# Kernel optimization log

Measured on AMD Instinct MI355X. Metric: run time of the kernel, lower is better.

## Reference

```python
import jax, jax.numpy as jnp
import numpy as np

B, T, D, H, L = 4, 2048, 256, 4, 2
HD = D // H
VOCAB, MAX_BITS, MLP_H = 32, 64, 64


def setup_inputs() -> dict:
    key = jax.random.key(0)
    ks = jax.random.split(key, 20)
    s = 0.02
    n = lambda k, shp: (jax.random.normal(k, shp, jnp.float32) * s)
    inp = {
        'tokens': jax.random.randint(ks[0], (B, T), 0, VOCAB),
        'embed': n(ks[1], (VOCAB, D)),
        'ln1_w': jnp.ones((L, D)), 'ln1_b': jnp.zeros((L, D)),
        'qkv_w': n(ks[2], (L, D, 3 * D)), 'qkv_b': jnp.zeros((L, 3 * D)),
        'proj_w': n(ks[3], (L, D, D)), 'proj_b': jnp.zeros((L, D)),
        'ln2_w': jnp.ones((L, D)), 'ln2_b': jnp.zeros((L, D)),
        'ffn1_w': n(ks[4], (L, D, 4 * D)), 'ffn1_b': jnp.zeros((L, 4 * D)),
        'ffn2_w': n(ks[5], (L, 4 * D, D)), 'ffn2_b': jnp.zeros((L, D)),
        'lnf_w': jnp.ones((D,)), 'lnf_b': jnp.zeros((D,)),
        'out_queries': n(ks[6], (MAX_BITS * 2, D)),
        'outp_w': n(ks[7], (D, 1)), 'outp_b': jnp.zeros((1,)),
        'mlp_w1': n(ks[8], (3, MLP_H)), 'mlp_b1': jnp.zeros((MLP_H,)),
        'mlp_w2': n(ks[9], (MLP_H, MLP_H)), 'mlp_b2': jnp.zeros((MLP_H,)),
        'mlp_w3': n(ks[10], (MLP_H, 2)), 'mlp_b3': jnp.zeros((2,)),
    }
    return inp


def _layernorm(x, w, b, eps=1e-5):
    mu = jnp.mean(x, axis=-1, keepdims=True)
    var = jnp.mean(jnp.square(x - mu), axis=-1, keepdims=True)
    return (x - mu) * jax.lax.rsqrt(var + eps) * w + b


def _rope_tables(t_len, hd):
    inv_freq = 1.0 / (10000.0 ** (jnp.arange(0, hd, 2, dtype=jnp.float32) / hd))
    freqs = jnp.outer(jnp.arange(t_len, dtype=jnp.float32), inv_freq)  # [T, hd/2]
    emb = jnp.concatenate([freqs, freqs], axis=-1)                     # [T, hd]
    return jnp.cos(emb)[None, :, None, :], jnp.sin(emb)[None, :, None, :]


def _rotate_half(x):
    x1, x2 = x[..., : x.shape[-1] // 2], x[..., x.shape[-1] // 2:]
    return jnp.concatenate([-x2, x1], axis=-1)


def _attention(x, qkv_w, qkv_b, proj_w, proj_b):
    b, t, c = x.shape
    qkv = (x @ qkv_w + qkv_b).reshape(b, t, 3, H, HD)
    q, k, v = qkv[:, :, 0], qkv[:, :, 1], qkv[:, :, 2]  # [B,T,H,HD]
    cos, sin = _rope_tables(t, HD)
    q = q * cos + _rotate_half(q) * sin
    k = k * cos + _rotate_half(k) * sin
    scores = jnp.einsum('bthd,bshd->bhts', q, k) / jnp.sqrt(jnp.float32(HD))
    causal = jnp.tril(jnp.ones((t, t), dtype=bool))
    scores = jnp.where(causal, scores, -jnp.inf)
    attn = jax.nn.softmax(scores, axis=-1)
    out = jnp.einsum('bhts,bshd->bthd', attn, v).reshape(b, t, c)
    return out @ proj_w + proj_b


def reference(tokens, embed, ln1_w, ln1_b, qkv_w, qkv_b, proj_w, proj_b,
              ln2_w, ln2_b, ffn1_w, ffn1_b, ffn2_w, ffn2_b, lnf_w, lnf_b,
              out_queries, outp_w, outp_b,
              mlp_w1, mlp_b1, mlp_w2, mlp_b2, mlp_w3, mlp_b3):
    x = embed[tokens]  # [B,T,D]
    for l in range(L):
        x = x + _attention(_layernorm(x, ln1_w[l], ln1_b[l]),
                           qkv_w[l], qkv_b[l], proj_w[l], proj_b[l])
        h = _layernorm(x, ln2_w[l], ln2_b[l])
        h = jax.nn.gelu(h @ ffn1_w[l] + ffn1_b[l], approximate=False)
        x = x + (h @ ffn2_w[l] + ffn2_b[l])
    x = _layernorm(x, lnf_w, lnf_b)
    # query cross-attention for bit-pair selection
    q_scores = jnp.einsum('qd,btd->bqt', out_queries, x) / jnp.sqrt(jnp.float32(D))
    q_attn = jax.nn.softmax(q_scores, axis=-1)           # [B, 2*MAX_BITS, T]
    selected = jnp.einsum('bqt,btd->bqd', q_attn, x)
    bits = jax.nn.sigmoid((selected @ outp_w + outp_b)[..., 0])
    pairs = bits.reshape(-1, MAX_BITS, 2)                # [B, MAX_BITS, 2]

    # sequential full-adder over bits
    def step(carry, ab):  # carry [B], ab [B,2]
        z = jnp.concatenate([ab, carry[:, None]], axis=-1)  # [B,3]
        h = jax.nn.relu(z @ mlp_w1 + mlp_b1)
        h = jax.nn.relu(h @ mlp_w2 + mlp_b2)
        o = jax.nn.sigmoid(h @ mlp_w3 + mlp_b3)
        return o[:, 1], o[:, 0]

    carry0 = jnp.zeros((pairs.shape[0],), jnp.float32)
    carry, sum_bits = jax.lax.scan(step, carry0, jnp.swapaxes(pairs, 0, 1))
    sum_all = jnp.concatenate([sum_bits.T, carry[:, None]], axis=1)  # [B, MAX_BITS+1]
    return sum_all, pairs, q_attn
```

## Files before the change

### kernel.cpp

```cpp
#include <hip/hip_runtime.h>
#include <hip/hip_bf16.h>

#define BB 4
#define TT 2048
#define DD 256
#define HH 4
#define HDD 64
#define NROW 8192
#define NQ 128

typedef __hip_bfloat16 bf16;
typedef __attribute__((ext_vector_type(8))) short bf8v;
typedef __attribute__((ext_vector_type(4))) short bf4v;
typedef __attribute__((ext_vector_type(4))) float f4v;

__device__ __forceinline__ bf16 f2b(float v){ return __float2bfloat16(v); }
__device__ __forceinline__ short f2bs(float v){
    bf16 h = __float2bfloat16(v);
    return *reinterpret_cast<short*>(&h);
}
__device__ __forceinline__ float bs2f(short s){
    bf16 h = *reinterpret_cast<bf16*>(&s);
    return __bfloat162float(h);
}
__device__ __forceinline__ float rl(float v, int l){
    return __uint_as_float(__builtin_amdgcn_readlane(__float_as_uint(v), l));
}

#define DPP_ROR_ADD(v, ctrl) \
    ((v) + __int_as_float(__builtin_amdgcn_update_dpp(0, __float_as_int(v), (ctrl), 0xF, 0xF, false)))

__device__ __forceinline__ float swap16_add(float v){
    float a = v, b = v;
    asm("v_permlane16_swap_b32 %0, %1" : "+v"(a), "+v"(b));
    return a + b;
}
__device__ __forceinline__ float swap32_add(float v){
    float a = v, b = v;
    asm("v_permlane32_swap_b32 %0, %1" : "+v"(a), "+v"(b));
    return a + b;
}

#define MFMA32(A,B,C) __builtin_amdgcn_mfma_f32_16x16x32_bf16((A),(B),(C),0,0,0)
#if __has_builtin(__builtin_amdgcn_mfma_f32_16x16x16bf16_1k)
#define MFMA16(A,B,C) __builtin_amdgcn_mfma_f32_16x16x16bf16_1k((A),(B),(C),0,0,0)
#else
__device__ __forceinline__ f4v mfma16_asm(bf4v a, bf4v b, f4v c){
    f4v d;
    asm("v_mfma_f32_16x16x16_bf16 %0, %1, %2, %3" : "=v"(d) : "v"(a), "v"(b), "v"(c));
    return d;
}
#define MFMA16(A,B,C) mfma16_asm((A),(B),(C))
#endif

__global__ __launch_bounds__(256) void k_embln(const int* __restrict__ tok,
                                               const float* __restrict__ emb,
                                               const float* __restrict__ w,
                                               const float* __restrict__ b,
                                               float* __restrict__ x,
                                               bf16* __restrict__ Y){
    __shared__ float red[256];
    int n = blockIdx.x, d = threadIdx.x;
    float v = emb[(long)tok[n]*DD + d];
    x[(long)n*DD + d] = v;
    red[d] = v; __syncthreads();
    for (int s=128; s>0; s>>=1){ if (d<s) red[d]+=red[d+s]; __syncthreads(); }
    float mu = red[0] * (1.0f/DD); __syncthreads();
    float df = v - mu;
    red[d] = df*df; __syncthreads();
    for (int s=128; s>0; s>>=1){ if (d<s) red[d]+=red[d+s]; __syncthreads(); }
    float var = red[0] * (1.0f/DD);
    Y[(long)n*DD + d] = f2b(df*rsqrtf(var+1e-5f)*w[d] + b[d]);
}

__global__ __launch_bounds__(256) void k_misc(const float* __restrict__ oq, bf16* __restrict__ oqb,
                                              float* __restrict__ cosT, float* __restrict__ sinT,
                                              const float* __restrict__ w2, float* __restrict__ w2t){
    int gid = blockIdx.x*256 + threadIdx.x;
    {
        int t = gid >> 5, dd = gid & 31;
        float invf = powf(10000.0f, -(float)(2*dd)/64.0f);
        float ang = (float)t * invf;
        float sn, cs;
        sincosf(ang, &sn, &cs);
        cosT[gid] = cs; sinT[gid] = sn;
    }
    if (gid < NQ*DD) oqb[gid] = f2b(oq[gid]);
    if (gid < 4096){ int j = gid >> 6, k = gid & 63; w2t[gid] = w2[k*64 + j]; }
}

__global__ __launch_bounds__(256) void k_wtall(const float* __restrict__ qkvw,
                                               const float* __restrict__ projw,
                                               const float* __restrict__ f1w,
                                               const float* __restrict__ f2w,
                                               bf16* __restrict__ wt){
    __shared__ float t[32][33];
    int z = blockIdx.z;
    int l = z >> 2, type = z & 3;
    long L = (long)l*786432;
    int K, M; const float* src; long doff;
    if (type == 0){ K=256;  M=768;  src = qkvw + (long)l*256*768;  doff = L; }
    else if (type == 1){ K=256;  M=256;  src = projw + (long)l*256*256; doff = L + 196608; }
    else if (type == 2){ K=256;  M=1024; src = f1w  + (long)l*256*1024; doff = L + 262144; }
    else               { K=1024; M=256;  src = f2w  + (long)l*1024*256; doff = L + 524288; }
    int m0 = blockIdx.x*32, k0 = blockIdx.y*32;
    if (m0 >= M || k0 >= K) return;
    bf16* dst = wt + doff;
    int tx = threadIdx.x, ty = threadIdx.y;
    #pragma unroll
    for (int i=0;i<4;i++)
        t[ty+i*8][tx] = src[(long)(k0+ty+i*8)*M + m0 + tx];
    __syncthreads();
    #pragma unroll
    for (int i=0;i<4;i++)
        dst[(long)(m0+ty+i*8)*K + k0 + tx] = f2b(t[tx][ty+i*8]);
}

__global__ __launch_bounds__(256) void k_lnb(const float* __restrict__ X,
                                             const float* __restrict__ w,
                                             const float* __restrict__ b,
                                             bf16* __restrict__ Y){
    __shared__ float red[256];
    int n = blockIdx.x, d = threadIdx.x;
    float v = X[(long)n*DD + d];
    red[d] = v; __syncthreads();
    for (int s=128; s>0; s>>=1){ if (d<s) red[d]+=red[d+s]; __syncthreads(); }
    float mu = red[0] * (1.0f/DD); __syncthreads();
    float df = v - mu;
    red[d] = df*df; __syncthreads();
    for (int s=128; s>0; s>>=1){ if (d<s) red[d]+=red[d+s]; __syncthreads(); }
    float var = red[0] * (1.0f/DD);
    Y[(long)n*DD + d] = f2b(df*rsqrtf(var+1e-5f)*w[d] + b[d]);
}

__global__ __launch_bounds__(256) void k_lnf(const float* __restrict__ X,
                                             const float* __restrict__ w,
                                             const float* __restrict__ b,
                                             const float* __restrict__ ow,
                                             bf16* __restrict__ Yb,
                                             float* __restrict__ g){
    __shared__ float red[256];
    int n = blockIdx.x, d = threadIdx.x;
    float v = X[(long)n*DD + d];
    red[d] = v; __syncthreads();
    for (int s=128; s>0; s>>=1){ if (d<s) red[d]+=red[d+s]; __syncthreads(); }
    float mu = red[0] * (1.0f/DD); __syncthreads();
    float df = v - mu;
    red[d] = df*df; __syncthreads();
    for (int s=128; s>0; s>>=1){ if (d<s) red[d]+=red[d+s]; __syncthreads(); }
    float var = red[0] * (1.0f/DD);
    float y = df*rsqrtf(var+1e-5f)*w[d] + b[d];
    Yb[(long)n*DD + d] = f2b(y);
    __syncthreads();
    red[d] = y * ow[d]; __syncthreads();
    for (int s=128; s>0; s>>=1){ if (d<s) red[d]+=red[d+s]; __syncthreads(); }
    if (d == 0) g[n] = red[0];
}

__global__ __launch_bounds__(256) void k_mgemm(const bf16* __restrict__ A,
                                               const bf16* __restrict__ Wt,
                                               const float* __restrict__ bias,
                                               float* __restrict__ Cf,
                                               bf16* __restrict__ Cb,
                                               int K, int M, int mode){
    __shared__ short As[128*32];
    __shared__ short Ws[64*32];
    int tid = threadIdx.x;
    int lane = tid & 63, wv = tid >> 6;
    int n0 = blockIdx.y * 128, m0 = blockIdx.x * 64;
    int rbase = (wv >> 1) * 64, cbase = (wv & 1) * 32;
    f4v acc[4][2] = {};
    int s2 = tid + 256;
    for (int k0 = 0; k0 < K; k0 += 32){
        bf8v va0 = *(const bf8v*)(A  + (long)(n0 + (tid>>2))*K + k0 + ((tid&3)<<3));
        bf8v va1 = *(const bf8v*)(A  + (long)(n0 + (s2 >>2))*K + k0 + ((s2 &3)<<3));
        bf8v vw  = *(const bf8v*)(Wt + (long)(m0 + (tid>>2))*K + k0 + ((tid&3)<<3));
        __syncthreads();
        *(bf8v*)&As[tid*8] = va0;
        *(bf8v*)&As[s2 *8] = va1;
        *(bf8v*)&Ws[tid*8] = vw;
        __syncthreads();
        bf8v af[4], bfr[2];
        int k8 = (lane >> 4) << 3;
        #pragma unroll
        for (int i=0;i<4;i++) af[i]  = *(bf8v*)&As[(rbase + i*16 + (lane&15))*32 + k8];
        #pragma unroll
        for (int j=0;j<2;j++) bfr[j] = *(bf8v*)&Ws[(cbase + j*16 + (lane&15))*32 + k8];
        #pragma unroll
        for (int i=0;i<4;i++)
            #pragma unroll
            for (int j=0;j<2;j++)
                acc[i][j] = MFMA32(af[i], bfr[j], acc[i][j]);
    }
    int rq = (lane >> 4) * 4;
    int cl = lane & 15;
    #pragma unroll
    for (int i=0;i<4;i++){
        #pragma unroll
        for (int j=0;j<2;j++){
            int m = m0 + cbase + j*16 + cl;
            float bs = bias[m];
            #pragma unroll
            for (int r=0;r<4;r++){
                int n = n0 + rbase + i*16 + rq + r;
                float v = acc[i][j][r] + bs;
                long idx = (long)n*M + m;
                if (mode == 0)      Cf[idx] = v;
                else if (mode == 1) Cf[idx] += v;
                else if (mode == 2) Cb[idx] = f2b(0.5f*v*(1.0f + erff(v*0.70710678118654752f)));
                else                Cb[idx] = f2b(v);
            }
        }
    }
}

__global__ __launch_bounds__(256) void k_mgemmQKV(const bf16* __restrict__ A,
                                                  const bf16* __restrict__ Wt,
                                                  const float* __restrict__ bias,
                                                  const float* __restrict__ cosT,
                                                  const float* __restrict__ sinT,
                                                  bf16* __restrict__ qb,
                                                  bf16* __restrict__ kb,
                                                  bf16* __restrict__ vt){
    __shared__ short As[128*32];
    __shared__ short Ws[64*32];
    __shared__ short E[128][68];
    const int K = 256, M = 768;
    int tid = threadIdx.x;
    int lane = tid & 63, wv = tid >> 6;
    int n0 = blockIdx.y * 128, m0 = blockIdx.x * 64;
    int rbase = (wv >> 1) * 64, cbase = (wv & 1) * 32;
    f4v acc[4][2] = {};
    int s2 = tid + 256;
    for (int k0 = 0; k0 < K; k0 += 32){
        bf8v va0 = *(const bf8v*)(A  + (long)(n0 + (tid>>2))*K + k0 + ((tid&3)<<3));
        bf8v va1 = *(const bf8v*)(A  + (long)(n0 + (s2 >>2))*K + k0 + ((s2 &3)<<3));
        bf8v vw  = *(const bf8v*)(Wt + (long)(m0 + (tid>>2))*K + k0 + ((tid&3)<<3));
        __syncthreads();
        *(bf8v*)&As[tid*8] = va0;
        *(bf8v*)&As[s2 *8] = va1;
        *(bf8v*)&Ws[tid*8] = vw;
        __syncthreads();
        bf8v af[4], bfr[2];
        int k8 = (lane >> 4) << 3;
        #pragma unroll
        for (int i=0;i<4;i++) af[i]  = *(bf8v*)&As[(rbase + i*16 + (lane&15))*32 + k8];
        #pragma unroll
        for (int j=0;j<2;j++) bfr[j] = *(bf8v*)&Ws[(cbase + j*16 + (lane&15))*32 + k8];
        #pragma unroll
        for (int i=0;i<4;i++)
            #pragma unroll
            for (int j=0;j<2;j++)
                acc[i][j] = MFMA32(af[i], bfr[j], acc[i][j]);
    }
    int rq = (lane >> 4) * 4;
    int cl = lane & 15;
    #pragma unroll
    for (int i=0;i<4;i++){
        #pragma unroll
        for (int j=0;j<2;j++){
            int cc = cbase + j*16 + cl;
            float bs = bias[m0 + cc];
            #pragma unroll
            for (int r=0;r<4;r++)
                E[rbase + i*16 + rq + r][cc] = f2bs(acc[i][j][r] + bs);
        }
    }
    __syncthreads();
    int part = m0 >> 8;
    int h = (m0 >> 6) & 3;
    int b = n0 >> 11;
    int t0 = n0 & 2047;
    int bh = b*HH + h;
    if (part < 2){
        bf16* dst0 = part ? kb : qb;
        int r2 = tid >> 2;
        int c0 = (tid & 3) * 16;
        int cpx = c0 ^ 32;
        #pragma unroll
        for (int half=0; half<2; half++){
            int row = half*64 + r2;
            int t = t0 + row;
            bf8v e0 = *(bf8v*)&E[row][c0];
            bf8v e1 = *(bf8v*)&E[row][c0+8];
            bf8v p0 = *(bf8v*)&E[row][cpx];
            bf8v p1 = *(bf8v*)&E[row][cpx+8];
            const float* ct = cosT + t*32;
            const float* st = sinT + t*32;
            short o[16];
            #pragma unroll
            for (int i=0;i<8;i++){
                int d = c0 + i, dd = d & 31;
                float cs = ct[dd], sn = st[dd];
                float v = bs2f(e0[i]), v2 = bs2f(p0[i]);
                o[i] = f2bs((d < 32) ? (v*cs - v2*sn) : (v*cs + v2*sn));
            }
            #pragma unroll
            for (int i=0;i<8;i++){
                int d = c0 + 8 + i, dd = d & 31;
                float cs = ct[dd], sn = st[dd];
                float v = bs2f(e1[i]), v2 = bs2f(p1[i]);
                o[8+i] = f2bs((d < 32) ? (v*cs - v2*sn) : (v*cs + v2*sn));
            }
            short* dp = (short*)dst0 + ((long)bh*TT + t)*64 + c0;
            *(bf8v*)dp     = *(bf8v*)&o[0];
            *(bf8v*)(dp+8) = *(bf8v*)&o[8];
        }
    } else {
        int tIdx0 = t0 >> 6;
        int d  = (tid & 127) >> 1;
        int k0 = (tid & 1) * 32;
        int tt = tid >> 7;
        short o[32];
        #pragma unroll
        for (int k=0;k<32;k++) o[k] = E[tt*64 + k0 + k][d];
        short* dp = (short*)vt + (((long)bh*32 + tIdx0 + tt)*64 + d)*64 + k0;
        *(bf8v*)dp      = *(bf8v*)&o[0];
        *(bf8v*)(dp+8)  = *(bf8v*)&o[8];
        *(bf8v*)(dp+16) = *(bf8v*)&o[16];
        *(bf8v*)(dp+24) = *(bf8v*)&o[24];
    }
}

__global__ __launch_bounds__(256) void k_fattn(const bf16* __restrict__ qb,
                                               const bf16* __restrict__ kb,
                                               const bf16* __restrict__ vt,
                                               bf16* __restrict__ ob){
    __shared__ short Ks[2][64][72];
    __shared__ short Vs[2][64][68];
    int bh = blockIdx.y;
    int qt = (int)(gridDim.x - 1) - (int)blockIdx.x;
    int tid = threadIdx.x;
    int lane = tid & 63, w = tid >> 6;
    int col = lane & 15, quad = lane >> 4;
    int q0 = qt*64 + w*16;
    const bf16* qp = qb + ((long)bh*TT + q0 + col)*64 + quad*8;
    bf8v bq0 = *(const bf8v*)(qp);
    bf8v bq1 = *(const bf8v*)(qp + 32);
    f4v oc[4] = {};
    float lsum = 0.f;
    int qglob = q0 + col;
    int srow = tid >> 2, sc0 = (tid & 3) * 16;
    const short* kgb = (const short*)kb + ((long)bh*TT + srow)*64 + sc0;
    const short* vgb = (const short*)vt + (((long)bh*32)*64 + srow)*64 + sc0;

    bf8v pk0 = *(const bf8v*)kgb;
    bf8v pk1 = *(const bf8v*)(kgb + 8);
    bf8v pv0 = *(const bf8v*)vgb;
    bf8v pv1 = *(const bf8v*)(vgb + 8);
    *(bf8v*)&Ks[0][srow][sc0]     = pk0;
    *(bf8v*)&Ks[0][srow][sc0 + 8] = pk1;
    *(bf8v*)&Vs[0][srow][sc0]     = pv0;
    *(bf8v*)&Vs[0][srow][sc0 + 8] = pv1;

    int buf = 0;
    for (int kt=0; kt<=qt; kt++){
        __syncthreads();
        bool more = (kt < qt);
        if (more){
            const short* kg = kgb + (long)(kt+1)*4096;
            const short* vg = vgb + (long)(kt+1)*4096;
            pk0 = *(const bf8v*)kg;
            pk1 = *(const bf8v*)(kg + 8);
            pv0 = *(const bf8v*)vg;
            pv1 = *(const bf8v*)(vg + 8);
        }
        bool diag = (kt == qt);
        int ntmax = diag ? w : 3;
        bf4v bp[4];
        #pragma unroll
        for (int nt=0; nt<4; nt++){
            if (nt > ntmax) continue;
            bf8v ka0 = *(const bf8v*)&Ks[buf][nt*16 + col][quad*8];
            bf8v ka1 = *(const bf8v*)&Ks[buf][nt*16 + col][32 + quad*8];
            f4v st = {};
            st = MFMA32(ka0, bq0, st);
            st = MFMA32(ka1, bq1, st);
            int key0 = kt*64 + nt*16 + quad*4;
            bf4v pb;
            #pragma unroll
            for (int r=0; r<4; r++){
                float e = __expf(st[r]*0.125f);
                if (diag && (key0 + r > qglob)) e = 0.f;
                lsum += e;
                pb[r] = f2bs(e);
            }
            bp[nt] = pb;
        }
        #pragma unroll
        for (int dt=0; dt<4; dt++){
            #pragma unroll
            for (int nt=0; nt<4; nt++){
                if (nt > ntmax) continue;
                bf4v va = *(const bf4v*)&Vs[buf][dt*16 + col][nt*16 + quad*4];
                oc[dt] = MFMA16(va, bp[nt], oc[dt]);
            }
        }
        if (more){
            *(bf8v*)&Ks[buf^1][srow][sc0]     = pk0;
            *(bf8v*)&Ks[buf^1][srow][sc0 + 8] = pk1;
            *(bf8v*)&Vs[buf^1][srow][sc0]     = pv0;
            *(bf8v*)&Vs[buf^1][srow][sc0 + 8] = pv1;
        }
        buf ^= 1;
    }
    lsum += __shfl_xor(lsum, 16, 64);
    lsum += __shfl_xor(lsum, 32, 64);
    float linv = 1.0f / lsum;

    int b = bh / HH, h = bh % HH;
    long obase = ((long)b*TT + q0 + col)*DD + h*64 + quad*4;
    #pragma unroll
    for (int dt=0; dt<4; dt++){
        bf4v o4;
        #pragma unroll
        for (int r=0; r<4; r++) o4[r] = f2bs(oc[dt][r]*linv);
        *(bf4v*)(ob + obase + dt*16) = o4;
    }
}

__global__ __launch_bounds__(256) void k_score(const bf16* __restrict__ oqb,
                                               const bf16* __restrict__ xfb,
                                               float* __restrict__ S){
    int b = blockIdx.y, t0 = blockIdx.x*64;
    int tid = threadIdx.x, lane = tid & 63, w = tid >> 6;
    int col = lane & 15, quad = lane >> 4, k8 = quad << 3;
    const bf16* xb = xfb + (long)b*TT*DD;
    f4v acc[2][4] = {};
    #pragma unroll
    for (int ko=0; ko<8; ko++){
        int kk = ko*32 + k8;
        bf8v a0 = *(const bf8v*)(oqb + (long)(w*32 +      col)*DD + kk);
        bf8v a1 = *(const bf8v*)(oqb + (long)(w*32 + 16 + col)*DD + kk);
        #pragma unroll
        for (int bt=0; bt<4; bt++){
            bf8v bv = *(const bf8v*)(xb + (long)(t0 + bt*16 + col)*DD + kk);
            acc[0][bt] = MFMA32(a0, bv, acc[0][bt]);
            acc[1][bt] = MFMA32(a1, bv, acc[1][bt]);
        }
    }
    #pragma unroll
    for (int qt2=0; qt2<2; qt2++){
        #pragma unroll
        for (int bt=0; bt<4; bt++){
            #pragma unroll
            for (int r=0; r<4; r++){
                int q = w*32 + qt2*16 + quad*4 + r;
                S[((long)b*NQ + q)*TT + t0 + bt*16 + col] = acc[qt2][bt][r]*0.0625f;
            }
        }
    }
}

__global__ __launch_bounds__(256) void k_psoft(const float* __restrict__ S,
                                               const float* __restrict__ g,
                                               const float* __restrict__ obias,
                                               float* __restrict__ out_qattn,
                                               float* __restrict__ out_pairs,
                                               float* __restrict__ bits){
    __shared__ float p[TT];
    __shared__ float red[256];
    int bq = blockIdx.x, b = bq >> 7;
    int tid = threadIdx.x;
    const float* Srow = S + (long)bq*TT;
    float lmax = -1e30f;
    for (int t=tid; t<TT; t+=256){ float s = Srow[t]; p[t] = s; lmax = fmaxf(lmax, s); }
    red[tid] = lmax; __syncthreads();
    for (int s2=128; s2>0; s2>>=1){ if (tid<s2) red[tid]=fmaxf(red[tid],red[tid+s2]); __syncthreads(); }
    float m = red[0]; __syncthreads();
    const float* gb = g + (long)b*TT;
    float lsum = 0.f, gdot = 0.f;
    for (int t=tid; t<TT; t+=256){
        float e = __expf(p[t]-m); p[t] = e;
        lsum += e; gdot += e*gb[t];
    }
    red[tid] = lsum; __syncthreads();
    for (int s2=128; s2>0; s2>>=1){ if (tid<s2) red[tid]+=red[tid+s2]; __syncthreads(); }
    float inv = 1.0f/red[0]; __syncthreads();
    red[tid] = gdot; __syncthreads();
    for (int s2=128; s2>0; s2>>=1){ if (tid<s2) red[tid]+=red[tid+s2]; __syncthreads(); }
    float gsum = red[0];
    for (int t=tid; t<TT; t+=256) out_qattn[(long)bq*TT + t] = p[t]*inv;
    if (tid == 0){
        float bit = 1.0f/(1.0f + expf(-(gsum*inv + obias[0])));
        bits[bq] = bit;
        out_pairs[bq] = bit;
    }
}

__global__ __launch_bounds__(64) void k_scan(const float* __restrict__ bits,
                                             const float* __restrict__ w1, const float* __restrict__ b1,
                                             const float* __restrict__ w2t, const float* __restrict__ b2,
                                             const float* __restrict__ w3, const float* __restrict__ b3,
                                             float* __restrict__ out_sum){
    __shared__ __align__(16) float h1s[64];
    int b = blockIdx.x, lane = threadIdx.x;
    float w1c0 = w1[lane], w1c1 = w1[64 + lane], w1c2 = w1[128 + lane];
    float b1v = b1[lane], b2v = b2[lane];
    float w3c0 = w3[lane*2 + 0], w3c1 = w3[lane*2 + 1];
    float b30 = b3[0], b31 = b3[1];
    const f4v* wrow = (const f4v*)(w2t + (long)lane*64);
    f4v c0v = wrow[0],  c1v = wrow[1],  c2v = wrow[2],  c3v = wrow[3],
        c4v = wrow[4],  c5v = wrow[5],  c6v = wrow[6],  c7v = wrow[7],
        c8v = wrow[8],  c9v = wrow[9],  cav = wrow[10], cbv = wrow[11],
        ccv = wrow[12], cdv = wrow[13], cev = wrow[14], cfv = wrow[15];
    float z0v = bits[b*128 + lane*2 + 0];
    float z1v = bits[b*128 + lane*2 + 1];
    const f4v* hv = (const f4v*)h1s;
    float carry = 0.f;
    for (int step=0; step<64; step++){
        float z0 = rl(z0v, step);
        float z1 = rl(z1v, step);
        float h1 = fmaxf(z0*w1c0 + z1*w1c1 + carry*w1c2 + b1v, 0.f);
        h1s[lane] = h1;
        __syncthreads();
        f4v va = hv[0]*c0v,  vb = hv[1]*c1v,  vc = hv[2]*c2v,   vd = hv[3]*c3v;
        va += hv[4]*c4v;   vb += hv[5]*c5v;   vc += hv[6]*c6v;   vd += hv[7]*c7v;
        va += hv[8]*c8v;   vb += hv[9]*c9v;   vc += hv[10]*cav;  vd += hv[11]*cbv;
        va += hv[12]*ccv;  vb += hv[13]*cdv;  vc += hv[14]*cev;  vd += hv[15]*cfv;
        __syncthreads();
        f4v vs = (va + vb) + (vc + vd);
        float h2 = fmaxf(((vs[0] + vs[1]) + (vs[2] + vs[3])) + b2v, 0.f);
        float t0 = h2*w3c0, t1 = h2*w3c1;
        t0 = DPP_ROR_ADD(t0, 0x121); t1 = DPP_ROR_ADD(t1, 0x121);
        t0 = DPP_ROR_ADD(t0, 0x122); t1 = DPP_ROR_ADD(t1, 0x122);
        t0 = DPP_ROR_ADD(t0, 0x124); t1 = DPP_ROR_ADD(t1, 0x124);
        t0 = DPP_ROR_ADD(t0, 0x128); t1 = DPP_ROR_ADD(t1, 0x128);
        t0 = swap16_add(t0); t1 = swap16_add(t1);
        t0 = swap32_add(t0); t1 = swap32_add(t1);
        float o0 = 1.0f/(1.0f + __expf(-(t0 + b30)));
        carry    = 1.0f/(1.0f + __expf(-(t1 + b31)));
        if (lane == 0) out_sum[b*65 + step] = o0;
    }
    if (lane == 0) out_sum[b*65 + 64] = carry;
}

extern "C" void kernel_launch(void* const* d_in, const int* in_sizes, int n_in,
                              void* d_out, int out_size, void* d_ws, size_t ws_size,
                              hipStream_t stream){
    const int*   tok   = (const int*)d_in[0];
    const float* emb   = (const float*)d_in[1];
    const float* ln1w  = (const float*)d_in[2];
    const float* ln1b  = (const float*)d_in[3];
    const float* qkvw  = (const float*)d_in[4];
    const float* qkvb  = (const float*)d_in[5];
    const float* projw = (const float*)d_in[6];
    const float* projb = (const float*)d_in[7];
    const float* ln2w  = (const float*)d_in[8];
    const float* ln2b  = (const float*)d_in[9];
    const float* f1w   = (const float*)d_in[10];
    const float* f1b   = (const float*)d_in[11];
    const float* f2w   = (const float*)d_in[12];
    const float* f2bb  = (const float*)d_in[13];
    const float* lnfw  = (const float*)d_in[14];
    const float* lnfb  = (const float*)d_in[15];
    const float* oq    = (const float*)d_in[16];
    const float* ow    = (const float*)d_in[17];
    const float* obias = (const float*)d_in[18];
    const float* w1    = (const float*)d_in[19];
    const float* b1    = (const float*)d_in[20];
    const float* w2    = (const float*)d_in[21];
    const float* b2    = (const float*)d_in[22];
    const float* w3    = (const float*)d_in[23];
    const float* b3    = (const float*)d_in[24];
    float* out = (float*)d_out;

    const long MB = 1048576;
    char* W = (char*)d_ws;
    float* x     = (float*)(W);
    bf16*  attnb = (bf16*)(W + 8*MB);
    bf16*  hb    = (bf16*)(W + 16*MB);
    bf16*  qb    = (bf16*)(W + 32*MB);
    bf16*  kb    = (bf16*)(W + 36*MB);
    bf16*  vt    = (bf16*)(W + 44*MB);
    bf16*  xnb   = (bf16*)(W + 48*MB);
    bf16*  wt    = (bf16*)(W + 52*MB);
    float* bits  = (float*)(W + 55*MB);
    bf16*  oqb   = (bf16*)(W + 56*MB);
    float* cosT  = (float*)(W + 57*MB);
    float* sinT  = cosT + 65536;
    float* w2t   = (float*)(W + 58*MB);
    bf16*  xfb   = (bf16*)(W + 32*MB);
    float* g     = (float*)(W + 36*MB);
    float* S     = (float*)(W + 40*MB);

    k_wtall<<<dim3(32, 32, 8), dim3(32,8), 0, stream>>>(qkvw, projw, f1w, f2w, wt);
    k_misc<<<256, 256, 0, stream>>>(oq, oqb, cosT, sinT, w2, w2t);

    k_embln<<<NROW, 256, 0, stream>>>(tok, emb, ln1w, ln1b, x, xnb);
    for (int l=0; l<2; l++){
        long L = (long)l*786432;
        if (l) k_lnb<<<NROW, 256, 0, stream>>>(x, ln1w + l*DD, ln1b + l*DD, xnb);
        k_mgemmQKV<<<dim3(768/64, 64), 256, 0, stream>>>(
            xnb, wt + L, qkvb + l*768, cosT, sinT, qb, kb, vt);
        k_fattn<<<dim3(TT/64, BB*HH), 256, 0, stream>>>(qb, kb, vt, attnb);
        k_mgemm<<<dim3(256/64, 64), 256, 0, stream>>>(
            attnb, wt + L + 196608, projb + l*DD, x, (bf16*)0, 256, 256, 1);
        k_lnb<<<NROW, 256, 0, stream>>>(x, ln2w + l*DD, ln2b + l*DD, xnb);
        k_mgemm<<<dim3(1024/64, 64), 256, 0, stream>>>(
            xnb, wt + L + 262144, f1b + l*1024, (float*)0, hb, 256, 1024, 2);
        k_mgemm<<<dim3(256/64, 64), 256, 0, stream>>>(
            hb, wt + L + 524288, f2bb + l*DD, x, (bf16*)0, 1024, 256, 1);
    }
    k_lnf<<<NROW, 256, 0, stream>>>(x, lnfw, lnfb, ow, xfb, g);
    k_score<<<dim3(TT/64, BB), 256, 0, stream>>>(oqb, xfb, S);
    k_psoft<<<BB*NQ, 256, 0, stream>>>(S, g, obias, out + 772, out + 260, bits);
    k_scan<<<4, 64, 0, stream>>>(bits, w1, b1, w2t, b2, w3, b3, out);
}
```

Before: 433.5 us.

## Replace shared-memory tree reductions with wave-level DPP reductions in LN and softmax

Rewrites the layernorm kernels to process one row per wavefront, using 4-wide vector loads and DPP/permlane wave reductions, with variance computed as E[x^2]-mu^2 in a single pass. This replaces the 256-thread block reductions and their many __syncthreads. The pooled softmax keeps the row in registers and reduces with wave primitives plus a small cross-wave shared array. The scan kernel double-buffers its hidden-state buffer so one barrier per step can be dropped. The one-pass variance formula is slightly less numerically robust than the two-pass version.

```diff
diff --git a/kernel.cpp b/kernel.cpp
--- a/kernel.cpp
+++ b/kernel.cpp
@@ -13,6 +13,7 @@
 typedef __attribute__((ext_vector_type(8))) short bf8v;
 typedef __attribute__((ext_vector_type(4))) short bf4v;
 typedef __attribute__((ext_vector_type(4))) float f4v;
+typedef __attribute__((ext_vector_type(2))) unsigned int u2v;
 
 __device__ __forceinline__ bf16 f2b(float v){ return __float2bfloat16(v); }
 __device__ __forceinline__ short f2bs(float v){
@@ -29,16 +30,44 @@
 
 #define DPP_ROR_ADD(v, ctrl) \
     ((v) + __int_as_float(__builtin_amdgcn_update_dpp(0, __float_as_int(v), (ctrl), 0xF, 0xF, false)))
-
-__device__ __forceinline__ float swap16_add(float v){
-    float a = v, b = v;
+#define DPP_ROR_MAX(v, ctrl) \
+    fmaxf((v), __int_as_float(__builtin_amdgcn_update_dpp(0, __float_as_int(v), (ctrl), 0xF, 0xF, false)))
+
+__device__ __forceinline__ void plswap16(float v, float& a, float& b){
+#if __has_builtin(__builtin_amdgcn_permlane16_swap)
+    u2v r = __builtin_amdgcn_permlane16_swap(__float_as_uint(v), __float_as_uint(v), false, false);
+    a = __uint_as_float(r.x); b = __uint_as_float(r.y);
+#else
+    a = v; b = v;
+    asm volatile("" : "+v"(b));
     asm("v_permlane16_swap_b32 %0, %1" : "+v"(a), "+v"(b));
-    return a + b;
-}
-__device__ __forceinline__ float swap32_add(float v){
-    float a = v, b = v;
+#endif
+}
+__device__ __forceinline__ void plswap32(float v, float& a, float& b){
+#if __has_builtin(__builtin_amdgcn_permlane32_swap)
+    u2v r = __builtin_amdgcn_permlane32_swap(__float_as_uint(v), __float_as_uint(v), false, false);
+    a = __uint_as_float(r.x); b = __uint_as_float(r.y);
+#else
+    a = v; b = v;
+    asm volatile("" : "+v"(b));
     asm("v_permlane32_swap_b32 %0, %1" : "+v"(a), "+v"(b));
-    return a + b;
+#endif
+}
+__device__ __forceinline__ float swap16_add(float v){ float a,b; plswap16(v,a,b); return a + b; }
+__device__ __forceinline__ float swap32_add(float v){ float a,b; plswap32(v,a,b); return a + b; }
+__device__ __forceinline__ float swap16_max(float v){ float a,b; plswap16(v,a,b); return fmaxf(a,b); }
+__device__ __forceinline__ float swap32_max(float v){ float a,b; plswap32(v,a,b); return fmaxf(a,b); }
+__device__ __forceinline__ float wsum(float v){
+    v = DPP_ROR_ADD(v, 0x121); v = DPP_ROR_ADD(v, 0x122);
+    v = DPP_ROR_ADD(v, 0x124); v = DPP_ROR_ADD(v, 0x128);
+    v = swap16_add(v); v = swap32_add(v);
+    return v;
+}
+__device__ __forceinline__ float wmax(float v){
+    v = DPP_ROR_MAX(v, 0x121); v = DPP_ROR_MAX(v, 0x122);
+    v = DPP_ROR_MAX(v, 0x124); v = DPP_ROR_MAX(v, 0x128);
+    v = swap16_max(v); v = swap32_max(v);
+    return v;
 }
 
 #define MFMA32(A,B,C) __builtin_amdgcn_mfma_f32_16x16x32_bf16((A),(B),(C),0,0,0)
@@ -59,18 +88,22 @@
                                                const float* __restrict__ b,
                                                float* __restrict__ x,
                                                bf16* __restrict__ Y){
-    __shared__ float red[256];
-    int n = blockIdx.x, d = threadIdx.x;
-    float v = emb[(long)tok[n]*DD + d];
-    x[(long)n*DD + d] = v;
-    red[d] = v; __syncthreads();
-    for (int s=128; s>0; s>>=1){ if (d<s) red[d]+=red[d+s]; __syncthreads(); }
-    float mu = red[0] * (1.0f/DD); __syncthreads();
-    float df = v - mu;
-    red[d] = df*df; __syncthreads();
-    for (int s=128; s>0; s>>=1){ if (d<s) red[d]+=red[d+s]; __syncthreads(); }
-    float var = red[0] * (1.0f/DD);
-    Y[(long)n*DD + d] = f2b(df*rsqrtf(var+1e-5f)*w[d] + b[d]);
+    int row = blockIdx.x*4 + (threadIdx.x >> 6);
+    int lane = threadIdx.x & 63;
+    f4v v = *(const f4v*)(emb + (long)tok[row]*DD + lane*4);
+    *(f4v*)(x + (long)row*DD + lane*4) = v;
+    float s  = (v[0]+v[1]) + (v[2]+v[3]);
+    float s2 = (v[0]*v[0]+v[1]*v[1]) + (v[2]*v[2]+v[3]*v[3]);
+    s = wsum(s); s2 = wsum(s2);
+    float mu  = s * (1.0f/DD);
+    float var = s2 * (1.0f/DD) - mu*mu;
+    float rs  = rsqrtf(var + 1e-5f);
+    f4v wv4 = *(const f4v*)(w + lane*4);
+    f4v bv4 = *(const f4v*)(b + lane*4);
+    bf4v o;
+    #pragma unroll
+    for (int i=0;i<4;i++) o[i] = f2bs((v[i]-mu)*rs*wv4[i] + bv4[i]);
+    *(bf4v*)(Y + (long)row*DD + lane*4) = o;
 }
 
 __global__ __launch_bounds__(256) void k_misc(const float* __restrict__ oq, bf16* __restrict__ oqb,
@@ -120,17 +153,21 @@
                                              const float* __restrict__ w,
                                              const float* __restrict__ b,
                                              bf16* __restrict__ Y){
-    __shared__ float red[256];
-    int n = blockIdx.x, d = threadIdx.x;
-    float v = X[(long)n*DD + d];
-    red[d] = v; __syncthreads();
-    for (int s=128; s>0; s>>=1){ if (d<s) red[d]+=red[d+s]; __syncthreads(); }
-    float mu = red[0] * (1.0f/DD); __syncthreads();
-    float df = v - mu;
-    red[d] = df*df; __syncthreads();
-    for (int s=128; s>0; s>>=1){ if (d<s) red[d]+=red[d+s]; __syncthreads(); }
-    float var = red[0] * (1.0f/DD);
-    Y[(long)n*DD + d] = f2b(df*rsqrtf(var+1e-5f)*w[d] + b[d]);
+    int row = blockIdx.x*4 + (threadIdx.x >> 6);
+    int lane = threadIdx.x & 63;
+    f4v v = *(const f4v*)(X + (long)row*DD + lane*4);
+    float s  = (v[0]+v[1]) + (v[2]+v[3]);
+    float s2 = (v[0]*v[0]+v[1]*v[1]) + (v[2]*v[2]+v[3]*v[3]);
+    s = wsum(s); s2 = wsum(s2);
+    float mu  = s * (1.0f/DD);
+    float var = s2 * (1.0f/DD) - mu*mu;
+    float rs  = rsqrtf(var + 1e-5f);
+    f4v wv4 = *(const f4v*)(w + lane*4);
+    f4v bv4 = *(const f4v*)(b + lane*4);
+    bf4v o;
+    #pragma unroll
+    for (int i=0;i<4;i++) o[i] = f2bs((v[i]-mu)*rs*wv4[i] + bv4[i]);
+    *(bf4v*)(Y + (long)row*DD + lane*4) = o;
 }
 
 __global__ __launch_bounds__(256) void k_lnf(const float* __restrict__ X,
@@ -139,22 +176,29 @@
                                              const float* __restrict__ ow,
                                              bf16* __restrict__ Yb,
                                              float* __restrict__ g){
-    __shared__ float red[256];
-    int n = blockIdx.x, d = threadIdx.x;
-    float v = X[(long)n*DD + d];
-    red[d] = v; __syncthreads();
-    for (int s=128; s>0; s>>=1){ if (d<s) red[d]+=red[d+s]; __syncthreads(); }
-    float mu = red[0] * (1.0f/DD); __syncthreads();
-    float df = v - mu;
-    red[d] = df*df; __syncthreads();
-    for (int s=128; s>0; s>>=1){ if (d<s) red[d]+=red[d+s]; __syncthreads(); }
-    float var = red[0] * (1.0f/DD);
-    float y = df*rsqrtf(var+1e-5f)*w[d] + b[d];
-    Yb[(long)n*DD + d] = f2b(y);
-    __syncthreads();
-    red[d] = y * ow[d]; __syncthreads();
-    for (int s=128; s>0; s>>=1){ if (d<s) red[d]+=red[d+s]; __syncthreads(); }
-    if (d == 0) g[n] = red[0];
+    int row = blockIdx.x*4 + (threadIdx.x >> 6);
+    int lane = threadIdx.x & 63;
+    f4v v = *(const f4v*)(X + (long)row*DD + lane*4);
+    float s  = (v[0]+v[1]) + (v[2]+v[3]);
+    float s2 = (v[0]*v[0]+v[1]*v[1]) + (v[2]*v[2]+v[3]*v[3]);
+    s = wsum(s); s2 = wsum(s2);
+    float mu  = s * (1.0f/DD);
+    float var = s2 * (1.0f/DD) - mu*mu;
+    float rs  = rsqrtf(var + 1e-5f);
+    f4v wv4 = *(const f4v*)(w + lane*4);
+    f4v bv4 = *(const f4v*)(b + lane*4);
+    f4v ov4 = *(const f4v*)(ow + lane*4);
+    bf4v o;
+    float gp = 0.f;
+    #pragma unroll
+    for (int i=0;i<4;i++){
+        float y = (v[i]-mu)*rs*wv4[i] + bv4[i];
+        o[i] = f2bs(y);
+        gp += y * ov4[i];
+    }
+    *(bf4v*)(Yb + (long)row*DD + lane*4) = o;
+    gp = wsum(gp);
+    if (lane == 0) g[row] = gp;
 }
 
 __global__ __launch_bounds__(256) void k_mgemm(const bf16* __restrict__ A,
@@ -458,31 +502,36 @@
                                                float* __restrict__ out_qattn,
                                                float* __restrict__ out_pairs,
                                                float* __restrict__ bits){
-    __shared__ float p[TT];
-    __shared__ float red[256];
+    __shared__ float cmax[4], cs[4], cg[4];
     int bq = blockIdx.x, b = bq >> 7;
-    int tid = threadIdx.x;
-    const float* Srow = S + (long)bq*TT;
-    float lmax = -1e30f;
-    for (int t=tid; t<TT; t+=256){ float s = Srow[t]; p[t] = s; lmax = fmaxf(lmax, s); }
-    red[tid] = lmax; __syncthreads();
-    for (int s2=128; s2>0; s2>>=1){ if (tid<s2) red[tid]=fmaxf(red[tid],red[tid+s2]); __syncthreads(); }
-    float m = red[0]; __syncthreads();
-    const float* gb = g + (long)b*TT;
-    float lsum = 0.f, gdot = 0.f;
-    for (int t=tid; t<TT; t+=256){
-        float e = __expf(p[t]-m); p[t] = e;
-        lsum += e; gdot += e*gb[t];
-    }
-    red[tid] = lsum; __syncthreads();
-    for (int s2=128; s2>0; s2>>=1){ if (tid<s2) red[tid]+=red[tid+s2]; __syncthreads(); }
-    float inv = 1.0f/red[0]; __syncthreads();
-    red[tid] = gdot; __syncthreads();
-    for (int s2=128; s2>0; s2>>=1){ if (tid<s2) red[tid]+=red[tid+s2]; __syncthreads(); }
-    float gsum = red[0];
-    for (int t=tid; t<TT; t+=256) out_qattn[(long)bq*TT + t] = p[t]*inv;
+    int tid = threadIdx.x, wv = tid >> 6, lane = tid & 63;
+    const f4v* S4 = (const f4v*)(S + (long)bq*TT);
+    f4v s0 = S4[tid], s1 = S4[tid + 256];
+    float lmax = fmaxf(fmaxf(fmaxf(s0[0],s0[1]), fmaxf(s0[2],s0[3])),
+                       fmaxf(fmaxf(s1[0],s1[1]), fmaxf(s1[2],s1[3])));
+    lmax = wmax(lmax);
+    if (lane == 0) cmax[wv] = lmax;
+    __syncthreads();
+    float m = fmaxf(fmaxf(cmax[0],cmax[1]), fmaxf(cmax[2],cmax[3]));
+    const f4v* g4 = (const f4v*)(g + (long)b*TT);
+    f4v gv0 = g4[tid], gv1 = g4[tid + 256];
+    f4v e0, e1;
+    #pragma unroll
+    for (int i=0;i<4;i++){ e0[i] = __expf(s0[i]-m); e1[i] = __expf(s1[i]-m); }
+    float lsum = (e0[0]+e0[1]+e0[2]+e0[3]) + (e1[0]+e1[1]+e1[2]+e1[3]);
+    float gdot = (e0[0]*gv0[0]+e0[1]*gv0[1]+e0[2]*gv0[2]+e0[3]*gv0[3])
+               + (e1[0]*gv1[0]+e1[1]*gv1[1]+e1[2]*gv1[2]+e1[3]*gv1[3]);
+    lsum = wsum(lsum); gdot = wsum(gdot);
+    if (lane == 0){ cs[wv] = lsum; cg[wv] = gdot; }
+    __syncthreads();
+    float Lr = (cs[0]+cs[1]) + (cs[2]+cs[3]);
+    float G  = (cg[0]+cg[1]) + (cg[2]+cg[3]);
+    float inv = 1.0f / Lr;
+    f4v* out4 = (f4v*)(out_qattn + (long)bq*TT);
+    out4[tid]       = e0 * inv;
+    out4[tid + 256] = e1 * inv;
     if (tid == 0){
-        float bit = 1.0f/(1.0f + expf(-(gsum*inv + obias[0])));
+        float bit = 1.0f/(1.0f + expf(-(G*inv + obias[0])));
         bits[bq] = bit;
         out_pairs[bq] = bit;
     }
@@ -493,7 +542,7 @@
                                              const float* __restrict__ w2t, const float* __restrict__ b2,
                                              const float* __restrict__ w3, const float* __restrict__ b3,
                                              float* __restrict__ out_sum){
-    __shared__ __align__(16) float h1s[64];
+    __shared__ __align__(16) float h1s[2][64];
     int b = blockIdx.x, lane = threadIdx.x;
     float w1c0 = w1[lane], w1c1 = w1[64 + lane], w1c2 = w1[128 + lane];
     float b1v = b1[lane], b2v = b2[lane];
@@ -506,19 +555,19 @@
         ccv = wrow[12], cdv = wrow[13], cev = wrow[14], cfv = wrow[15];
     float z0v = bits[b*128 + lane*2 + 0];
     float z1v = bits[b*128 + lane*2 + 1];
-    const f4v* hv = (const f4v*)h1s;
     float carry = 0.f;
     for (int step=0; step<64; step++){
         float z0 = rl(z0v, step);
         float z1 = rl(z1v, step);
         float h1 = fmaxf(z0*w1c0 + z1*w1c1 + carry*w1c2 + b1v, 0.f);
-        h1s[lane] = h1;
+        float* hb = h1s[step & 1];
+        hb[lane] = h1;
         __syncthreads();
+        const f4v* hv = (const f4v*)hb;
         f4v va = hv[0]*c0v,  vb = hv[1]*c1v,  vc = hv[2]*c2v,   vd = hv[3]*c3v;
         va += hv[4]*c4v;   vb += hv[5]*c5v;   vc += hv[6]*c6v;   vd += hv[7]*c7v;
         va += hv[8]*c8v;   vb += hv[9]*c9v;   vc += hv[10]*cav;  vd += hv[11]*cbv;
         va += hv[12]*ccv;  vb += hv[13]*cdv;  vc += hv[14]*cev;  vd += hv[15]*cfv;
-        __syncthreads();
         f4v vs = (va + vb) + (vc + vd);
         float h2 = fmaxf(((vs[0] + vs[1]) + (vs[2] + vs[3])) + b2v, 0.f);
         float t0 = h2*w3c0, t1 = h2*w3c1;
@@ -587,22 +636,22 @@
     k_wtall<<<dim3(32, 32, 8), dim3(32,8), 0, stream>>>(qkvw, projw, f1w, f2w, wt);
     k_misc<<<256, 256, 0, stream>>>(oq, oqb, cosT, sinT, w2, w2t);
 
-    k_embln<<<NROW, 256, 0, stream>>>(tok, emb, ln1w, ln1b, x, xnb);
+    k_embln<<<NROW/4, 256, 0, stream>>>(tok, emb, ln1w, ln1b, x, xnb);
     for (int l=0; l<2; l++){
         long L = (long)l*786432;
-        if (l) k_lnb<<<NROW, 256, 0, stream>>>(x, ln1w + l*DD, ln1b + l*DD, xnb);
+        if (l) k_lnb<<<NROW/4, 256, 0, stream>>>(x, ln1w + l*DD, ln1b + l*DD, xnb);
         k_mgemmQKV<<<dim3(768/64, 64), 256, 0, stream>>>(
             xnb, wt + L, qkvb + l*768, cosT, sinT, qb, kb, vt);
         k_fattn<<<dim3(TT/64, BB*HH), 256, 0, stream>>>(qb, kb, vt, attnb);
         k_mgemm<<<dim3(256/64, 64), 256, 0, stream>>>(
             attnb, wt + L + 196608, projb + l*DD, x, (bf16*)0, 256, 256, 1);
-        k_lnb<<<NROW, 256, 0, stream>>>(x, ln2w + l*DD, ln2b + l*DD, xnb);
+        k_lnb<<<NROW/4, 256, 0, stream>>>(x, ln2w + l*DD, ln2b + l*DD, xnb);
         k_mgemm<<<dim3(1024/64, 64), 256, 0, stream>>>(
             xnb, wt + L + 262144, f1b + l*1024, (float*)0, hb, 256, 1024, 2);
         k_mgemm<<<dim3(256/64, 64), 256, 0, stream>>>(
             hb, wt + L + 524288, f2bb + l*DD, x, (bf16*)0, 1024, 256, 1);
     }
-    k_lnf<<<NROW, 256, 0, stream>>>(x, lnfw, lnfb, ow, xfb, g);
+    k_lnf<<<NROW/4, 256, 0, stream>>>(x, lnfw, lnfb, ow, xfb, g);
     k_score<<<dim3(TT/64, BB), 256, 0, stream>>>(oqb, xfb, S);
     k_psoft<<<BB*NQ, 256, 0, stream>>>(S, g, obias, out + 772, out + 260, bits);
     k_scan<<<4, 64, 0, stream>>>(bits, w1, b1, w2t, b2, w3, b3, out);
```

New measurement: 397.7 us. 1.09x faster.
